# Performance work log

Hardware: AMD Instinct MI355X
Metric: run time of the kernel (lower is better)

## Reference

```python
import jax, jax.numpy as jnp
import numpy as np

T = 10          # time_steps
IN_DIM = 784    # 28*28
HID = 256
NCLS = 47
THRESH = 1.0
TAU_MEM = 2.0   # LIF membrane time constant
TAU_OUT = 2.0   # readout EMA time constant


@jax.custom_vjp
def spike_fn(u):
    # Heaviside spike on (v - threshold), surrogate gradient in bwd.
    return (u >= 0.0).astype(u.dtype)

def _spike_fwd(u):
    return spike_fn(u), u

def _spike_bwd(u, g):
    # sigmoid surrogate derivative, slope 4
    s = jax.nn.sigmoid(4.0 * u)
    return (g * 4.0 * s * (1.0 - s),)

spike_fn.defvjp(_spike_fwd, _spike_bwd)


def setup_inputs() -> dict:
    key = jax.random.key(0)
    k1, k2, k3 = jax.random.split(key, 3)
    x = jax.random.uniform(k1, (4096, 1, 28, 28), dtype=jnp.float32)
    W1 = jax.random.normal(k2, (IN_DIM, HID), dtype=jnp.float32) / np.float32(np.sqrt(IN_DIM))
    b1 = jnp.zeros((HID,), jnp.float32)
    Wr = jax.random.normal(k3, (HID, NCLS), dtype=jnp.float32) / np.float32(np.sqrt(HID))
    br = jnp.zeros((NCLS,), jnp.float32)
    return {"x": x, "W1": W1, "b1": b1, "Wr": Wr, "br": br}


def reference(x, W1, b1, Wr, br):
    B = x.shape[0]
    xf = x.reshape(B, -1)  # [B, 784] pixel intensities in [0,1]
    # rate_encode_flat: Bernoulli(p=pixel) spikes per timestep -> [T, B, 784]
    ek = jax.random.key(42)
    seq = (jax.random.uniform(ek, (T, B, IN_DIM), dtype=xf.dtype) < xf[None]).astype(xf.dtype)

    def step(carry, s_t):
        v_hid, v_out = carry
        I_hid = s_t @ W1 + b1                      # [B, HID]
        v_hid = v_hid + (I_hid - v_hid) / TAU_MEM  # leaky integration
        spk = spike_fn(v_hid - THRESH)             # spike emission
        v_hid = v_hid * (1.0 - spk)                # hard reset to 0
        I = spk @ Wr + br                          # [B, NCLS]
        v_out = v_out + (I - v_out) / TAU_OUT      # output EMA
        return (v_hid, v_out), None

    init = (jnp.zeros((B, HID), xf.dtype), jnp.zeros((B, NCLS), xf.dtype))
    (_, v_out), _ = jax.lax.scan(step, init, seq)
    return v_out
```

## Files before the change

### kernel.cpp

```cpp
#include <hip/hip_runtime.h>
#include <stdint.h>


#define T_STEPS 10
#define BATCH   4096
#define IN_DIM  784
#define HID     256
#define NCLS    47
#define NROWS   (T_STEPS * BATCH)
#define KWORDS  25
#define KPAD    800
#define M_TILE  160

#define WS_IALL_OFF 0u
#define WS_W1HI_OFF 46039040u
#define WS_W1MD_OFF (46039040u + 409600u)
#define WS_W1LO_OFF (46039040u + 819200u)

typedef __attribute__((ext_vector_type(8))) short    bf16x8;
typedef __attribute__((ext_vector_type(4))) float    f32x4;
typedef __attribute__((ext_vector_type(4))) uint32_t u32x4;

__device__ __forceinline__ uint32_t rotl32(uint32_t x, uint32_t r) {
    return __builtin_amdgcn_alignbit(x, x, 32u - r);
}

__device__ __forceinline__ uint32_t tf_hash(uint32_t lo) {
    const uint32_t ks1 = 42u;
    const uint32_t ks2 = 0x1BD11BDAu ^ 42u;
    uint32_t x0 = 0u;
    uint32_t x1 = lo + ks1;
#define TF_RND(r) { x0 += x1; x1 = rotl32(x1, r); x1 ^= x0; }
    TF_RND(13) TF_RND(15) TF_RND(26) TF_RND(6)
    x0 += ks1; x1 += ks2 + 1u;
    TF_RND(17) TF_RND(29) TF_RND(16) TF_RND(24)
    x0 += ks2; x1 += 2u;
    TF_RND(13) TF_RND(15) TF_RND(26) TF_RND(6)
    x1 += ks1 + 3u;
    TF_RND(17) TF_RND(29) TF_RND(16) TF_RND(24)
    x0 += ks1; x1 += ks2 + 4u;
    TF_RND(13) TF_RND(15) TF_RND(26) TF_RND(6)
    x0 += ks2; x1 += 5u;
#undef TF_RND
    return x0 ^ x1;
}

__device__ __forceinline__ uint32_t hash2(uint32_t ib, const float* xp) {
    float2 xx = *(const float2*)xp;
    uint32_t w = 0u;
    w |= ((float)(tf_hash(ib + 0u) >> 9) < xx.x * 8388608.0f) ? 0x3F80u : 0u;
    w |= ((float)(tf_hash(ib + 1u) >> 9) < xx.y * 8388608.0f) ? 0x3F800000u : 0u;
    return w;
}

__global__ __launch_bounds__(256) void splitk_k(
        const float* __restrict__ W1, ushort* __restrict__ hiT,
        ushort* __restrict__ midT, ushort* __restrict__ loT) {
    int n = blockIdx.x;
    for (int k = threadIdx.x; k < KPAD; k += 256) {
        float w = (k < IN_DIM) ? W1[k * HID + n] : 0.0f;
        uint32_t u = __float_as_uint(w);
        uint32_t hb = (u + 0x7FFFu + ((u >> 16) & 1u)) >> 16;
        float hf = __uint_as_float(hb << 16);
        float r1 = w - hf;
        uint32_t u1 = __float_as_uint(r1);
        uint32_t mb = (u1 + 0x7FFFu + ((u1 >> 16) & 1u)) >> 16;
        float mf2 = __uint_as_float(mb << 16);
        float r2 = r1 - mf2;
        uint32_t u2 = __float_as_uint(r2);
        uint32_t lb = (u2 + 0x7FFFu + ((u2 >> 16) & 1u)) >> 16;
        hiT [n * KPAD + k] = (ushort)hb;
        midT[n * KPAD + k] = (ushort)mb;
        loT [n * KPAD + k] = (ushort)lb;
    }
}

#define LDS_B0  20480
#define B_BUFSZ 49152
#define A_BUFSZ 10240

__global__ __launch_bounds__(512, 1) void fused_gemm_k(
        const ushort* __restrict__ hiT, const ushort* __restrict__ midT,
        const ushort* __restrict__ loT, const float* __restrict__ b1,
        const float* __restrict__ x, float* __restrict__ I_all) {
    __shared__ __align__(16) char lds[118784];

    const int tid = threadIdx.x;
    const int l   = tid & 63;
    const int wv  = tid >> 6;
    const int wm  = wv >> 2;
    const int wn  = wv & 3;
    const int m0  = blockIdx.x * M_TILE;

    f32x4 acc[5][4] = {};

    const int q   = l >> 4;
    const int sig = q ^ (l & 3) ^ ((l >> 2) & 3);
    const int a_rd = wm * 5120 + ((l & 15) << 6) + (sig << 4);
    const int b_rd = (((wn << 6) + (l & 15)) << 6) + (sig << 4);

    const ushort* hi_p[2];
    const ushort* md_p[2];
    const ushort* lo_p[2];
    int bdst[2];
#pragma unroll
    for (int i = 0; i < 2; ++i) {
        int s  = (i << 9) + tid;
        int n  = s >> 2;
        int qs = s & 3;
        int qd = qs ^ (n & 3) ^ ((n >> 2) & 3);
        size_t eoff = (size_t)n * KPAD + ((size_t)qd << 3);
        hi_p[i] = hiT  + eoff;
        md_p[i] = midT + eoff;
        lo_p[i] = loT  + eoff;
        bdst[i] = ((i << 9) + (wv << 6)) << 4;
    }

    int      adst[5];
    const float* txp[5];
    uint32_t tib[5];
    int      tpp[5];
#pragma unroll
    for (int s = 0; s < 5; ++s) {
        int tau = tid + (s << 9);
        int row = tau >> 4;
        int p   = tau & 15;
        int qd  = (p >> 2) ^ (row & 3) ^ ((row >> 2) & 3);
        adst[s] = (row << 6) + (qd << 4) + ((p & 3) << 2);
        int rowg = m0 + row;
        txp[s]  = x + (size_t)(rowg & (BATCH - 1)) * IN_DIM + (p << 1);
        tib[s]  = (uint32_t)rowg * (uint32_t)IN_DIM + (uint32_t)(p << 1);
        tpp[s]  = p;
    }

#define STAGE_B(koff, bbase) \
    _Pragma("unroll") \
    for (int i = 0; i < 2; ++i) { \
        __builtin_amdgcn_global_load_lds( \
            (const __attribute__((address_space(1))) void*)(hi_p[i] + (koff)), \
            (__attribute__((address_space(3))) void*)(lds + (bbase) + bdst[i]), \
            16, 0, 0); \
        __builtin_amdgcn_global_load_lds( \
            (const __attribute__((address_space(1))) void*)(md_p[i] + (koff)), \
            (__attribute__((address_space(3))) void*)(lds + (bbase) + 16384 + bdst[i]), \
            16, 0, 0); \
        __builtin_amdgcn_global_load_lds( \
            (const __attribute__((address_space(1))) void*)(lo_p[i] + (koff)), \
            (__attribute__((address_space(3))) void*)(lds + (bbase) + 32768 + bdst[i]), \
            16, 0, 0); \
    }

#define HASH_TASK(s, koff, abase, is_tail) { \
    uint32_t w_ = 0u; \
    if (!(is_tail) || tpp[s] < 8) \
        w_ = hash2(tib[s] + (uint32_t)(koff), txp[s] + (koff)); \
    *(uint32_t*)(lds + (abase) + adst[s]) = w_; }

#define MFMA_CHUNK(s) \
    _Pragma("unroll") \
    for (int m = (s) * 12; m < (s) * 12 + 12; ++m) { \
        const int nt_ = m / 15, r_ = m % 15, pl_ = r_ / 5, mt_ = r_ % 5; \
        acc[mt_][nt_] = __builtin_amdgcn_mfma_f32_16x16x32_bf16( \
            af[mt_], bfr[pl_][nt_], acc[mt_][nt_], 0, 0, 0); \
    }

#define PRELOAD_FRAGS(bufidx) \
    const char* A = lds + (bufidx) * A_BUFSZ; \
    const char* B = lds + LDS_B0 + (bufidx) * B_BUFSZ; \
    bf16x8 af[5]; \
    bf16x8 bfr[3][4]; \
    _Pragma("unroll") \
    for (int mt = 0; mt < 5; ++mt) \
        af[mt] = *(const bf16x8*)(A + a_rd + (mt << 10)); \
    _Pragma("unroll") \
    for (int nt = 0; nt < 4; ++nt) { \
        bfr[0][nt] = *(const bf16x8*)(B + b_rd + (nt << 10)); \
        bfr[1][nt] = *(const bf16x8*)(B + 16384 + b_rd + (nt << 10)); \
        bfr[2][nt] = *(const bf16x8*)(B + 32768 + b_rd + (nt << 10)); \
    }

    STAGE_B(0, LDS_B0)
    HASH_TASK(0, 0, 0, false)
    HASH_TASK(1, 0, 0, false)
    HASH_TASK(2, 0, 0, false)
    HASH_TASK(3, 0, 0, false)
    HASH_TASK(4, 0, 0, false)
    __syncthreads();

    int cur = 0;
#pragma unroll 1
    for (int kw = 0; kw < KWORDS - 1; ++kw) {
        const int  nxt  = cur ^ 1;
        const int  koff = (kw + 1) << 5;
        const bool tail = (kw == KWORDS - 2);

        STAGE_B(koff, LDS_B0 + nxt * B_BUFSZ)

        PRELOAD_FRAGS(cur)

        const int ab = nxt * A_BUFSZ;
        HASH_TASK(0, koff, ab, tail)  MFMA_CHUNK(0)
        HASH_TASK(1, koff, ab, tail)  MFMA_CHUNK(1)
        HASH_TASK(2, koff, ab, tail)  MFMA_CHUNK(2)
        HASH_TASK(3, koff, ab, tail)  MFMA_CHUNK(3)
        HASH_TASK(4, koff, ab, tail)  MFMA_CHUNK(4)

        __syncthreads();
        cur = nxt;
    }

    {
        PRELOAD_FRAGS(cur)
        MFMA_CHUNK(0) MFMA_CHUNK(1) MFMA_CHUNK(2) MFMA_CHUNK(3) MFMA_CHUNK(4)
    }
#undef STAGE_B
#undef HASH_TASK
#undef MFMA_CHUNK
#undef PRELOAD_FRAGS

    const int c0 = l & 15;
    float b1v[4];
#pragma unroll
    for (int nt = 0; nt < 4; ++nt)
        b1v[nt] = b1[(wn << 6) + (nt << 4) + c0];
#pragma unroll
    for (int mt = 0; mt < 5; ++mt) {
#pragma unroll
        for (int nt = 0; nt < 4; ++nt) {
            int col = (wn << 6) + (nt << 4) + c0;
#pragma unroll
            for (int r = 0; r < 4; ++r) {
                int row = m0 + wm * 80 + (mt << 4) + (q << 2) + r;
                I_all[(size_t)row * HID + col] = acc[mt][nt][r] + b1v[nt];
            }
        }
    }
}

__global__ __launch_bounds__(256) void scanout_k(
        const float* __restrict__ I_all, const float* __restrict__ Wr,
        const float* __restrict__ br, float* __restrict__ out) {
    __shared__ float gl[4 * 256];
    const int tid = threadIdx.x;
    const int b0  = blockIdx.x << 2;

#pragma unroll
    for (int b = 0; b < 4; ++b) {
        const float* p = I_all + ((size_t)(b0 + b) << 8) + tid;
        float v = 0.f, ga = 0.f, wt = 0.0009765625f;
#pragma unroll
        for (int t = 0; t < T_STEPS; ++t) {
            float I = p[(size_t)t * BATCH * HID];
            v = v + (I - v) * 0.5f;
            if (v >= 1.0f) { ga += wt; v = 0.f; }
            wt += wt;
        }
        gl[(b << 8) + tid] = ga;
    }
    __syncthreads();

    const int wv = tid >> 6;
    const int c  = tid & 63;
    if (c >= NCLS) return;
    const float* gb = &gl[wv << 8];
    float acc = 0.f;
    for (int h4 = 0; h4 < 64; ++h4) {
        float w0 = Wr[((h4 << 2) + 0) * NCLS + c];
        float w1 = Wr[((h4 << 2) + 1) * NCLS + c];
        float w2 = Wr[((h4 << 2) + 2) * NCLS + c];
        float w3 = Wr[((h4 << 2) + 3) * NCLS + c];
        float4 gg = *(const float4*)&gb[h4 << 2];
        acc = fmaf(gg.x, w0, acc);
        acc = fmaf(gg.y, w1, acc);
        acc = fmaf(gg.z, w2, acc);
        acc = fmaf(gg.w, w3, acc);
    }
    float brv = br[c] * 0.9990234375f;
    out[(b0 + wv) * NCLS + c] = acc + brv;
}

extern "C" void kernel_launch(void* const* d_in, const int* in_sizes, int n_in,
                              void* d_out, int out_size, void* d_ws, size_t ws_size,
                              hipStream_t stream) {
    const float* x  = (const float*)d_in[0];
    const float* W1 = (const float*)d_in[1];
    const float* b1 = (const float*)d_in[2];
    const float* Wr = (const float*)d_in[3];
    const float* br = (const float*)d_in[4];
    float* out = (float*)d_out;

    float*  I_all = (float*) ((char*)d_ws + WS_IALL_OFF);
    ushort* w1hi  = (ushort*)((char*)d_ws + WS_W1HI_OFF);
    ushort* w1md  = (ushort*)((char*)d_ws + WS_W1MD_OFF);
    ushort* w1lo  = (ushort*)((char*)d_ws + WS_W1LO_OFF);

    splitk_k<<<HID, 256, 0, stream>>>(W1, w1hi, w1md, w1lo);
    fused_gemm_k<<<NROWS / M_TILE, 512, 0, stream>>>(w1hi, w1md, w1lo, b1, x, I_all);
    scanout_k<<<BATCH / 4, 256, 0, stream>>>(I_all, Wr, br, out);
}
```

Baseline: 186.8 us.

## Fuse LIF scan and readout into GEMM epilogue by tiling rows by batch

Each GEMM block now covers 16 batch rows across all 10 time steps instead of 160 consecutive flattened rows. The membrane scan and the Wr readout then run in the epilogue through LDS. This removes the 40 MB I_all round trip through global memory and the separate scanout kernel launch. The cost is a serialized epilogue: one half of the warps stages time steps 0-4 in LDS, the other half runs the scan, and the readout loop per block is small and poorly parallel.

```diff
diff --git a/kernel.cpp b/kernel.cpp
--- a/kernel.cpp
+++ b/kernel.cpp
@@ -12,7 +12,6 @@
 #define KPAD    800
 #define M_TILE  160
 
-#define WS_IALL_OFF 0u
 #define WS_W1HI_OFF 46039040u
 #define WS_W1MD_OFF (46039040u + 409600u)
 #define WS_W1LO_OFF (46039040u + 819200u)
@@ -78,11 +77,15 @@
 #define LDS_B0  20480
 #define B_BUFSZ 49152
 #define A_BUFSZ 10240
+#define I0_LDW  258
+#define G_LDW   260
+#define G_OFF   83200
 
 __global__ __launch_bounds__(512, 1) void fused_gemm_k(
         const ushort* __restrict__ hiT, const ushort* __restrict__ midT,
         const ushort* __restrict__ loT, const float* __restrict__ b1,
-        const float* __restrict__ x, float* __restrict__ I_all) {
+        const float* __restrict__ x, const float* __restrict__ Wr,
+        const float* __restrict__ br, float* __restrict__ out) {
     __shared__ __align__(16) char lds[118784];
 
     const int tid = threadIdx.x;
@@ -90,7 +93,7 @@
     const int wv  = tid >> 6;
     const int wm  = wv >> 2;
     const int wn  = wv & 3;
-    const int m0  = blockIdx.x * M_TILE;
+    const int b0  = blockIdx.x << 4;
 
     f32x4 acc[5][4] = {};
 
@@ -127,8 +130,8 @@
         int p   = tau & 15;
         int qd  = (p >> 2) ^ (row & 3) ^ ((row >> 2) & 3);
         adst[s] = (row << 6) + (qd << 4) + ((p & 3) << 2);
-        int rowg = m0 + row;
-        txp[s]  = x + (size_t)(rowg & (BATCH - 1)) * IN_DIM + (p << 1);
+        int rowg = ((row >> 4) * BATCH) + b0 + (row & 15);
+        txp[s]  = x + (size_t)(b0 + (row & 15)) * IN_DIM + (p << 1);
         tib[s]  = (uint32_t)rowg * (uint32_t)IN_DIM + (uint32_t)(p << 1);
         tpp[s]  = p;
     }
@@ -195,7 +198,6 @@
         const bool tail = (kw == KWORDS - 2);
 
         STAGE_B(koff, LDS_B0 + nxt * B_BUFSZ)
-
         PRELOAD_FRAGS(cur)
 
         const int ab = nxt * A_BUFSZ;
@@ -223,60 +225,78 @@
 #pragma unroll
     for (int nt = 0; nt < 4; ++nt)
         b1v[nt] = b1[(wn << 6) + (nt << 4) + c0];
-#pragma unroll
-    for (int mt = 0; mt < 5; ++mt) {
+
+    __syncthreads();
+    float* i0   = (float*)lds;
+    float* gbuf = (float*)(lds + G_OFF);
+
+    if (wm == 0) {
+#pragma unroll
+        for (int mt = 0; mt < 5; ++mt)
+#pragma unroll
+            for (int nt = 0; nt < 4; ++nt) {
+                int col = (wn << 6) + (nt << 4) + c0;
+#pragma unroll
+                for (int r = 0; r < 4; ++r) {
+                    int j = (q << 2) + r;
+                    i0[(mt * 16 + j) * I0_LDW + col] = acc[mt][nt][r] + b1v[nt];
+                }
+            }
+    }
+    __syncthreads();
+
+    if (wm == 1) {
 #pragma unroll
         for (int nt = 0; nt < 4; ++nt) {
             int col = (wn << 6) + (nt << 4) + c0;
 #pragma unroll
             for (int r = 0; r < 4; ++r) {
-                int row = m0 + wm * 80 + (mt << 4) + (q << 2) + r;
-                I_all[(size_t)row * HID + col] = acc[mt][nt][r] + b1v[nt];
+                int j = (q << 2) + r;
+                float v = 0.f, ga = 0.f, wt = 0.0009765625f;
+#pragma unroll
+                for (int t = 0; t < 5; ++t) {
+                    float I = i0[(t * 16 + j) * I0_LDW + col];
+                    v = v + (I - v) * 0.5f;
+                    if (v >= 1.0f) { ga += wt; v = 0.f; }
+                    wt += wt;
+                }
+#pragma unroll
+                for (int mt = 0; mt < 5; ++mt) {
+                    float I = acc[mt][nt][r] + b1v[nt];
+                    v = v + (I - v) * 0.5f;
+                    if (v >= 1.0f) { ga += wt; v = 0.f; }
+                    wt += wt;
+                }
+                gbuf[j * G_LDW + col] = ga;
             }
         }
     }
-}
-
-__global__ __launch_bounds__(256) void scanout_k(
-        const float* __restrict__ I_all, const float* __restrict__ Wr,
-        const float* __restrict__ br, float* __restrict__ out) {
-    __shared__ float gl[4 * 256];
-    const int tid = threadIdx.x;
-    const int b0  = blockIdx.x << 2;
-
-#pragma unroll
-    for (int b = 0; b < 4; ++b) {
-        const float* p = I_all + ((size_t)(b0 + b) << 8) + tid;
-        float v = 0.f, ga = 0.f, wt = 0.0009765625f;
-#pragma unroll
-        for (int t = 0; t < T_STEPS; ++t) {
-            float I = p[(size_t)t * BATCH * HID];
-            v = v + (I - v) * 0.5f;
-            if (v >= 1.0f) { ga += wt; v = 0.f; }
-            wt += wt;
+    __syncthreads();
+
+    {
+        const int c = l;
+        if (c < NCLS) {
+            float brv = br[c] * 0.9990234375f;
+#pragma unroll
+            for (int rr = 0; rr < 2; ++rr) {
+                int j = (wv << 1) + rr;
+                const float* gb = &gbuf[j * G_LDW];
+                float a = 0.f;
+                for (int h4 = 0; h4 < 64; ++h4) {
+                    float w0 = Wr[((h4 << 2) + 0) * NCLS + c];
+                    float w1 = Wr[((h4 << 2) + 1) * NCLS + c];
+                    float w2 = Wr[((h4 << 2) + 2) * NCLS + c];
+                    float w3 = Wr[((h4 << 2) + 3) * NCLS + c];
+                    float4 gg = *(const float4*)&gb[h4 << 2];
+                    a = fmaf(gg.x, w0, a);
+                    a = fmaf(gg.y, w1, a);
+                    a = fmaf(gg.z, w2, a);
+                    a = fmaf(gg.w, w3, a);
+                }
+                out[(b0 + j) * NCLS + c] = a + brv;
+            }
         }
-        gl[(b << 8) + tid] = ga;
-    }
-    __syncthreads();
-
-    const int wv = tid >> 6;
-    const int c  = tid & 63;
-    if (c >= NCLS) return;
-    const float* gb = &gl[wv << 8];
-    float acc = 0.f;
-    for (int h4 = 0; h4 < 64; ++h4) {
-        float w0 = Wr[((h4 << 2) + 0) * NCLS + c];
-        float w1 = Wr[((h4 << 2) + 1) * NCLS + c];
-        float w2 = Wr[((h4 << 2) + 2) * NCLS + c];
-        float w3 = Wr[((h4 << 2) + 3) * NCLS + c];
-        float4 gg = *(const float4*)&gb[h4 << 2];
-        acc = fmaf(gg.x, w0, acc);
-        acc = fmaf(gg.y, w1, acc);
-        acc = fmaf(gg.z, w2, acc);
-        acc = fmaf(gg.w, w3, acc);
-    }
-    float brv = br[c] * 0.9990234375f;
-    out[(b0 + wv) * NCLS + c] = acc + brv;
+    }
 }
 
 extern "C" void kernel_launch(void* const* d_in, const int* in_sizes, int n_in,
@@ -289,12 +309,11 @@
     const float* br = (const float*)d_in[4];
     float* out = (float*)d_out;
 
-    float*  I_all = (float*) ((char*)d_ws + WS_IALL_OFF);
     ushort* w1hi  = (ushort*)((char*)d_ws + WS_W1HI_OFF);
     ushort* w1md  = (ushort*)((char*)d_ws + WS_W1MD_OFF);
     ushort* w1lo  = (ushort*)((char*)d_ws + WS_W1LO_OFF);
 
     splitk_k<<<HID, 256, 0, stream>>>(W1, w1hi, w1md, w1lo);
-    fused_gemm_k<<<NROWS / M_TILE, 512, 0, stream>>>(w1hi, w1md, w1lo, b1, x, I_all);
-    scanout_k<<<BATCH / 4, 256, 0, stream>>>(I_all, Wr, br, out);
-}
+    fused_gemm_k<<<BATCH / 16, 512, 0, stream>>>(w1hi, w1md, w1lo, b1, x,
+                                                 Wr, br, out);
+}
```

New measurement: 171.8 us. -8.0%, faster.
